# Kernel optimization log

Hardware: AMD Instinct MI355X
Metric: run time of the kernel (lower is better)

The kernel has to match this reference:

```python
import jax, jax.numpy as jnp
import numpy as np

H = 1024
W = 1024
N = 128
K1 = 21.7  # on-road exponential loss scale
K2 = 40.0  # off-road exponential loss scale


def setup_inputs() -> dict:
    key = jax.random.key(0)
    k1, k2 = jax.random.split(key)
    hd_map = (jax.random.uniform(k1, (H, W)) < 0.3).astype(jnp.float32)
    # integer pixel coordinates, kept away from the border so the 2x2
    # neighbor window is always in-bounds (matches typical usage)
    prediction = jax.random.randint(k2, (N, 2), 2, H - 2).astype(jnp.int32)
    return {"hd_map": hd_map, "prediction": prediction}


def reference(hd_map, prediction):
    Hm, Wm = hd_map.shape
    p = prediction.astype(jnp.float32)  # [N,2]

    # Separable squared distances from each point to every pixel.
    # NOTE: faithful to the original, nonzero()[:,0] (row) is compared with
    # point[0] and nonzero()[:,1] (col) with point[1].
    rows = jnp.arange(Hm, dtype=jnp.float32)
    cols = jnp.arange(Wm, dtype=jnp.float32)
    dr2 = (rows[None, :] - p[:, 0:1]) ** 2  # [N,H]
    dc2 = (cols[None, :] - p[:, 1:2]) ** 2  # [N,W]
    d2 = dr2[:, :, None] + dc2[:, None, :]  # [N,H,W]

    INF = jnp.float32(1e30)
    on_mask = hd_map != 0  # nonzero pixels of hd_map (non-drivable)
    # min squared distance to nearest nonzero pixel of hd_map
    d2_on = jnp.min(jnp.where(on_mask[None], d2, INF), axis=(1, 2))  # [N]
    # min squared distance to nearest nonzero pixel of (1 - hd_map)
    d2_off = jnp.min(jnp.where(on_mask[None], INF, d2), axis=(1, 2))  # [N]

    px = prediction[:, 0]
    py = prediction[:, 1]
    # is_outside_frame: point[0] vs shape[0], point[1] vs shape[1] (faithful)
    outside_frame = (px < 0) | (px > Hm) | (py < 0) | (py > Wm)

    # is_outside_road: 2x2 window im[py-1:py+1, px-1:px+1] contains a 1
    ir = jnp.stack([py - 1, py - 1, py, py], axis=-1)  # [N,4]
    ic = jnp.stack([px - 1, px, px - 1, px], axis=-1)  # [N,4]
    neigh = hd_map[ir, ic]  # [N,4]
    outside_road = jnp.any(neigh == 1.0, axis=-1)

    ln2 = jnp.log(jnp.float32(2.0))
    # off-road: exp(d * ln(2)/k2); on-road: exp(-d^2 / k1)
    loss_off = jnp.exp(jnp.sqrt(d2_off) * (ln2 / K2))
    loss_on = jnp.exp(-d2_on / K1)

    per_point = jnp.where(
        outside_frame,
        jnp.float32(0.0),
        jnp.where(outside_road, loss_off, loss_on),
    )
    return jnp.mean(per_point)
```

## Files before the change

### kernel.cpp

```cpp
#include <hip/hip_runtime.h>
#include <math.h>

#define HMAP 1024
#define WMAP 1024
#define NPTS 128

__device__ __forceinline__ int clampi(int x, int hi) {
    return x < 0 ? 0 : (x > hi ? hi : x);
}

__global__ __launch_bounds__(128)
void roadloss_kernel(const float* __restrict__ hd_map,
                     const int* __restrict__ pred,
                     int n,
                     float* __restrict__ out) {
    __shared__ float smem[128];
    int t = threadIdx.x;
    float per_point = 0.0f;

    if (t < n) {
        int px = pred[2 * t];
        int py = pred[2 * t + 1];

        float best_on  = 1e30f;
        float best_off = 1e30f;

        if (px >= 0 && px < HMAP && py >= 0 && py < WMAP) {
            float v = hd_map[px * WMAP + py];
            if (v != 0.0f) best_on = 0.0f; else best_off = 0.0f;
        }

        for (int k = 1; k <= 2048; ++k) {
            float fk  = (float)k;
            float dk2 = fk * fk;

            {
                float nk2 = fk * fk;
                if (best_on <= nk2 && best_off <= nk2) break;
            }

            int c0 = py - k, c1 = py + k;
            int cs = clampi(c0, WMAP - 1);
            int ce = clampi(c1, WMAP - 1);
            if (c0 < 0) cs = 0;
            if (c1 > WMAP - 1) ce = WMAP - 1;
            if (c0 > WMAP - 1 || c1 < 0) { cs = 1; ce = 0; }

            int rt = px - k;
            if (rt >= 0 && rt < HMAP) {
                const float* rowp = hd_map + rt * WMAP;
                for (int c = cs; c <= ce; ++c) {
                    float dc = (float)(c - py);
                    float d2 = dk2 + dc * dc;
                    float v = rowp[c];
                    if (v != 0.0f) best_on = fminf(best_on, d2);
                    else           best_off = fminf(best_off, d2);
                }
            }
            int rb = px + k;
            if (rb >= 0 && rb < HMAP) {
                const float* rowp = hd_map + rb * WMAP;
                for (int c = cs; c <= ce; ++c) {
                    float dc = (float)(c - py);
                    float d2 = dk2 + dc * dc;
                    float v = rowp[c];
                    if (v != 0.0f) best_on = fminf(best_on, d2);
                    else           best_off = fminf(best_off, d2);
                }
            }

            int r0 = px - k + 1, r1 = px + k - 1;
            int rs = r0 < 0 ? 0 : r0;
            int re = r1 > HMAP - 1 ? HMAP - 1 : r1;
            int cl = py - k;
            if (cl >= 0 && cl < WMAP) {
                for (int r = rs; r <= re; ++r) {
                    float dr = (float)(r - px);
                    float d2 = dr * dr + dk2;
                    float v = hd_map[r * WMAP + cl];
                    if (v != 0.0f) best_on = fminf(best_on, d2);
                    else           best_off = fminf(best_off, d2);
                }
            }
            int cr = py + k;
            if (cr >= 0 && cr < WMAP) {
                for (int r = rs; r <= re; ++r) {
                    float dr = (float)(r - px);
                    float d2 = dr * dr + dk2;
                    float v = hd_map[r * WMAP + cr];
                    if (v != 0.0f) best_on = fminf(best_on, d2);
                    else           best_off = fminf(best_off, d2);
                }
            }
        }

        bool outside_frame = (px < 0) || (px > HMAP) || (py < 0) || (py > WMAP);

        int r0c = clampi(py - 1, HMAP - 1);
        int r1c = clampi(py,     HMAP - 1);
        int c0c = clampi(px - 1, WMAP - 1);
        int c1c = clampi(px,     WMAP - 1);
        bool outside_road =
            (hd_map[r0c * WMAP + c0c] == 1.0f) ||
            (hd_map[r0c * WMAP + c1c] == 1.0f) ||
            (hd_map[r1c * WMAP + c0c] == 1.0f) ||
            (hd_map[r1c * WMAP + c1c] == 1.0f);

        const float K1 = 21.7f;
        const float K2 = 40.0f;
        const float LN2 = 0.6931471805599453f;
        float loss_off = expf(sqrtf(best_off) * (LN2 / K2));
        float loss_on  = expf(-best_on / K1);
        per_point = outside_frame ? 0.0f : (outside_road ? loss_off : loss_on);
    }

    smem[t] = per_point;
    __syncthreads();
    for (int s = 64; s > 0; s >>= 1) {
        if (t < s) smem[t] = smem[t] + smem[t + s];
        __syncthreads();
    }
    if (t == 0) out[0] = smem[0] / (float)n;
}

extern "C" void kernel_launch(void* const* d_in, const int* in_sizes, int n_in,
                              void* d_out, int out_size, void* d_ws, size_t ws_size,
                              hipStream_t stream) {
    const float* hd_map = (const float*)d_in[0];
    const int*   pred   = (const int*)d_in[1];
    float* out = (float*)d_out;
    int n = in_sizes[1] / 2;
    roadloss_kernel<<<1, 128, 0, stream>>>(hd_map, pred, n, out);
}
```

Before: 62.19 us.

## Parallelize nearest-pixel search with one wavefront per point and a fixed window

```diff
diff --git a/kernel.cpp b/kernel.cpp
--- a/kernel.cpp
+++ b/kernel.cpp
@@ -3,124 +3,88 @@
 
 #define HMAP 1024
 #define WMAP 1024
-#define NPTS 128
 
 __device__ __forceinline__ int clampi(int x, int hi) {
     return x < 0 ? 0 : (x > hi ? hi : x);
 }
 
-__global__ __launch_bounds__(128)
-void roadloss_kernel(const float* __restrict__ hd_map,
-                     const int* __restrict__ pred,
-                     int n,
-                     float* __restrict__ out) {
-    __shared__ float smem[128];
-    int t = threadIdx.x;
-    float per_point = 0.0f;
+__global__ __launch_bounds__(64)
+void roadloss_scan(const float* __restrict__ hd_map,
+                   const int* __restrict__ pred,
+                   int n,
+                   float* __restrict__ out,
+                   float* __restrict__ ws) {
+    const int pt   = blockIdx.x;
+    const int lane = threadIdx.x;
+    const int px = pred[2 * pt];
+    const int py = pred[2 * pt + 1];
 
-    if (t < n) {
-        int px = pred[2 * t];
-        int py = pred[2 * t + 1];
+    const int r0c = clampi(py - 1, HMAP - 1), r1c = clampi(py, HMAP - 1);
+    const int c0c = clampi(px - 1, WMAP - 1), c1c = clampi(px, WMAP - 1);
+    const float n00 = hd_map[r0c * WMAP + c0c];
+    const float n01 = hd_map[r0c * WMAP + c1c];
+    const float n10 = hd_map[r1c * WMAP + c0c];
+    const float n11 = hd_map[r1c * WMAP + c1c];
 
-        float best_on  = 1e30f;
-        float best_off = 1e30f;
+    float best_on = 1e30f, best_off = 1e30f;
 
-        if (px >= 0 && px < HMAP && py >= 0 && py < WMAP) {
-            float v = hd_map[px * WMAP + py];
-            if (v != 0.0f) best_on = 0.0f; else best_off = 0.0f;
-        }
-
-        for (int k = 1; k <= 2048; ++k) {
-            float fk  = (float)k;
-            float dk2 = fk * fk;
-
-            {
-                float nk2 = fk * fk;
-                if (best_on <= nk2 && best_off <= nk2) break;
-            }
-
-            int c0 = py - k, c1 = py + k;
-            int cs = clampi(c0, WMAP - 1);
-            int ce = clampi(c1, WMAP - 1);
-            if (c0 < 0) cs = 0;
-            if (c1 > WMAP - 1) ce = WMAP - 1;
-            if (c0 > WMAP - 1 || c1 < 0) { cs = 1; ce = 0; }
-
-            int rt = px - k;
-            if (rt >= 0 && rt < HMAP) {
-                const float* rowp = hd_map + rt * WMAP;
-                for (int c = cs; c <= ce; ++c) {
-                    float dc = (float)(c - py);
-                    float d2 = dk2 + dc * dc;
-                    float v = rowp[c];
-                    if (v != 0.0f) best_on = fminf(best_on, d2);
-                    else           best_off = fminf(best_off, d2);
-                }
-            }
-            int rb = px + k;
-            if (rb >= 0 && rb < HMAP) {
-                const float* rowp = hd_map + rb * WMAP;
-                for (int c = cs; c <= ce; ++c) {
-                    float dc = (float)(c - py);
-                    float d2 = dk2 + dc * dc;
-                    float v = rowp[c];
-                    if (v != 0.0f) best_on = fminf(best_on, d2);
-                    else           best_off = fminf(best_off, d2);
-                }
-            }
-
-            int r0 = px - k + 1, r1 = px + k - 1;
-            int rs = r0 < 0 ? 0 : r0;
-            int re = r1 > HMAP - 1 ? HMAP - 1 : r1;
-            int cl = py - k;
-            if (cl >= 0 && cl < WMAP) {
-                for (int r = rs; r <= re; ++r) {
-                    float dr = (float)(r - px);
-                    float d2 = dr * dr + dk2;
-                    float v = hd_map[r * WMAP + cl];
-                    if (v != 0.0f) best_on = fminf(best_on, d2);
-                    else           best_off = fminf(best_off, d2);
-                }
-            }
-            int cr = py + k;
-            if (cr >= 0 && cr < WMAP) {
-                for (int r = rs; r <= re; ++r) {
-                    float dr = (float)(r - px);
-                    float d2 = dr * dr + dk2;
-                    float v = hd_map[r * WMAP + cr];
-                    if (v != 0.0f) best_on = fminf(best_on, d2);
-                    else           best_off = fminf(best_off, d2);
-                }
+    const int R = 16;
+#pragma unroll
+    for (int ii = 0; ii < 18; ++ii) {
+        int i = lane + ii * 64;
+        if (i < 33 * 33) {
+            int dr = i / 33 - R;
+            int dc = i % 33 - R;
+            int r = px + dr, c = py + dc;
+            if ((unsigned)r < (unsigned)HMAP && (unsigned)c < (unsigned)WMAP) {
+                float v  = hd_map[r * WMAP + c];
+                float d2 = (float)(dr * dr + dc * dc);
+                if (v != 0.0f) best_on  = fminf(best_on,  d2);
+                else           best_off = fminf(best_off, d2);
             }
         }
-
-        bool outside_frame = (px < 0) || (px > HMAP) || (py < 0) || (py > WMAP);
-
-        int r0c = clampi(py - 1, HMAP - 1);
-        int r1c = clampi(py,     HMAP - 1);
-        int c0c = clampi(px - 1, WMAP - 1);
-        int c1c = clampi(px,     WMAP - 1);
-        bool outside_road =
-            (hd_map[r0c * WMAP + c0c] == 1.0f) ||
-            (hd_map[r0c * WMAP + c1c] == 1.0f) ||
-            (hd_map[r1c * WMAP + c0c] == 1.0f) ||
-            (hd_map[r1c * WMAP + c1c] == 1.0f);
-
-        const float K1 = 21.7f;
-        const float K2 = 40.0f;
-        const float LN2 = 0.6931471805599453f;
-        float loss_off = expf(sqrtf(best_off) * (LN2 / K2));
-        float loss_on  = expf(-best_on / K1);
-        per_point = outside_frame ? 0.0f : (outside_road ? loss_off : loss_on);
+    }
+#pragma unroll
+    for (int s = 1; s < 64; s <<= 1) {
+        best_on  = fminf(best_on,  __shfl_xor(best_on,  s, 64));
+        best_off = fminf(best_off, __shfl_xor(best_off, s, 64));
     }
 
-    smem[t] = per_point;
-    __syncthreads();
-    for (int s = 64; s > 0; s >>= 1) {
-        if (t < s) smem[t] = smem[t] + smem[t + s];
-        __syncthreads();
+    const float guard = (float)((R + 1) * (R + 1));
+    if (!(best_on <= guard && best_off <= guard)) {
+        for (int i = lane; i < HMAP * WMAP; i += 64) {
+            int r = i >> 10, c = i & (WMAP - 1);
+            int dri = r - px, dci = c - py;
+            float d2 = (float)(dri * dri + dci * dci);
+            float v = hd_map[i];
+            if (v != 0.0f) best_on  = fminf(best_on,  d2);
+            else           best_off = fminf(best_off, d2);
+        }
+#pragma unroll
+        for (int s = 1; s < 64; s <<= 1) {
+            best_on  = fminf(best_on,  __shfl_xor(best_on,  s, 64));
+            best_off = fminf(best_off, __shfl_xor(best_off, s, 64));
+        }
     }
-    if (t == 0) out[0] = smem[0] / (float)n;
+
+    if (lane == 0) {
+        bool outside_frame = (px < 0) | (px > HMAP) | (py < 0) | (py > WMAP);
+        bool outside_road  = (n00 == 1.0f) | (n01 == 1.0f) |
+                             (n10 == 1.0f) | (n11 == 1.0f);
+        const float K1 = 21.7f, K2 = 40.0f;
+        const float LN2 = 0.6931471805599453f;
+        float loss = outside_frame
+                         ? 0.0f
+                         : (outside_road ? expf(sqrtf(best_off) * (LN2 / K2))
+                                         : expf(-best_on / K1));
+        atomicAdd(&ws[0], loss);
+        __threadfence();
+        unsigned old = atomicAdd((unsigned int*)(ws + 1), 1u);
+        if (old == (unsigned)(n - 1)) {
+            float total = atomicAdd(&ws[0], 0.0f);
+            out[0] = total / (float)n;
+        }
+    }
 }
 
 extern "C" void kernel_launch(void* const* d_in, const int* in_sizes, int n_in,
@@ -129,6 +93,9 @@
     const float* hd_map = (const float*)d_in[0];
     const int*   pred   = (const int*)d_in[1];
     float* out = (float*)d_out;
+    float* ws  = (float*)d_ws;
     int n = in_sizes[1] / 2;
-    roadloss_kernel<<<1, 128, 0, stream>>>(hd_map, pred, n, out);
+
+    hipMemsetAsync(ws, 0, 2 * sizeof(float), stream);
+    roadloss_scan<<<n, 64, 0, stream>>>(hd_map, pred, n, out, ws);
 }
```

Result: slower. 65.17 us (+4.8%).
